# Kernel optimization log

Measured on AMD Instinct MI355X. Metric: run time of the kernel, lower is better.

The kernel has to match this reference:

```python
import jax, jax.numpy as jnp
import numpy as np

# ---- model hyperparameters (match init_kwargs) ----
D_MODEL = 1024
D_STATE = 128
EXPAND = 2
HEADDIM = 64
NGROUPS = 1
D_INNER = EXPAND * D_MODEL            # 2048
NHEADS = D_INNER // HEADDIM           # 32
ROPE_FRAC = 0.5
SPLIT = int(D_STATE * ROPE_FRAC)      # 64 rotary dims
NANG = SPLIT // 2                     # 32 rope angles
A_FLOOR = 1e-4
EPS = 1e-5
BATCH, SEQLEN = 1, 1024
SIZES = [D_INNER, D_INNER, D_STATE * NGROUPS, D_STATE * NGROUPS, NHEADS, NHEADS, NHEADS, NANG]
D_IN_PROJ = int(np.sum(SIZES))        # 4480


def setup_inputs() -> dict:
    key = jax.random.key(0)
    ks = jax.random.split(key, 6)
    u = jax.random.normal(ks[0], (BATCH, SEQLEN, D_MODEL), dtype=jnp.float32)
    W_in = jax.random.normal(ks[1], (D_MODEL, D_IN_PROJ), dtype=jnp.float32) * 0.02
    # dt_bias ~ log(dt) for dt in [1e-3, 0.1] -> around -4
    dt_bias = jax.random.normal(ks[2], (NHEADS,), dtype=jnp.float32) * 0.5 - 4.0
    B_bias = jnp.ones((NHEADS, D_STATE), jnp.float32) + 0.01 * jax.random.normal(ks[3], (NHEADS, D_STATE), dtype=jnp.float32)
    C_bias = jnp.ones((NHEADS, D_STATE), jnp.float32) + 0.01 * jax.random.normal(ks[4], (NHEADS, D_STATE), dtype=jnp.float32)
    Bn_w = jnp.ones((D_STATE,), jnp.float32)
    Cn_w = jnp.ones((D_STATE,), jnp.float32)
    D_param = jnp.ones((NHEADS,), jnp.float32)
    W_out = jax.random.normal(ks[5], (D_INNER, D_MODEL), dtype=jnp.float32) * 0.02
    return {"u": u, "W_in": W_in, "dt_bias": dt_bias, "B_bias": B_bias, "C_bias": C_bias,
            "Bn_w": Bn_w, "Cn_w": Cn_w, "D_param": D_param, "W_out": W_out}


def _rmsnorm(v, w):
    return v * jax.lax.rsqrt(jnp.mean(v * v, axis=-1, keepdims=True) + EPS) * w


def _forward(u, W_in, dt_bias, B_bias, C_bias, Bn_w, Cn_w, D_param, W_out):
    b, l, _ = u.shape
    proj = u @ W_in                                   # (b, l, d_in_proj)
    idx = np.cumsum(SIZES)[:-1]
    z, x, Bp, Cp, dd_dt, dd_A, trap_raw, ang = jnp.split(proj, idx, axis=-1)
    z = z.reshape(b, l, NHEADS, HEADDIM)
    x = x.reshape(b, l, NHEADS, HEADDIM)
    # A = clamp(-softplus(.), max=-A_floor);  dt = softplus(. + dt_bias)
    A = jnp.minimum(-jax.nn.softplus(dd_A), -A_FLOOR)          # (b,l,H)
    dt = jax.nn.softplus(dd_dt + dt_bias)                      # (b,l,H)
    a = jnp.exp(A * dt)                                        # decay per step
    lam = jax.nn.sigmoid(trap_raw)                             # trapezoid gate
    # RMSNorm on B/C (ngroups=1), then per-head additive bias
    Bn = _rmsnorm(Bp, Bn_w)                                    # (b,l,N)
    Cn = _rmsnorm(Cp, Cn_w)
    Bh = Bn[:, :, None, :] + B_bias                            # (b,l,H,N)
    Ch = Cn[:, :, None, :] + C_bias
    # data-dependent rotary: cumulative angle = cumsum(angles * dt)
    theta = jnp.cumsum(ang[:, :, None, :] * dt[..., None], axis=1)  # (b,l,H,NANG)
    cos, sin = jnp.cos(theta), jnp.sin(theta)

    def rope(v):
        d1, d2, rest = v[..., :NANG], v[..., NANG:SPLIT], v[..., SPLIT:]
        return jnp.concatenate([d1 * cos - d2 * sin, d1 * sin + d2 * cos, rest], axis=-1)

    Bh, Ch = rope(Bh), rope(Ch)

    tfirst = lambda v: jnp.moveaxis(v, 1, 0)
    inputs = (tfirst(Bh), tfirst(Ch), tfirst(x), tfirst(a), tfirst(dt), tfirst(lam))
    h0 = jnp.zeros((b, NHEADS, HEADDIM, D_STATE), jnp.float32)
    k0 = jnp.zeros((b, NHEADS, D_STATE), jnp.float32)
    v0 = jnp.zeros((b, NHEADS, HEADDIM), jnp.float32)

    def step(carry, inp):
        h, kp, vp = carry
        Bt, Ct, xt, at, dtt, lamt = inp
        # trapezoidal selective-scan update:
        # h_t = a_t h_{t-1} + dt_t (lam_t B_t x_t + (1-lam_t) a_t B_{t-1} x_{t-1})
        cur = jnp.einsum('bhp,bhn->bhpn', xt, Bt) * (dtt * lamt)[..., None, None]
        prv = jnp.einsum('bhp,bhn->bhpn', vp, kp) * (dtt * (1.0 - lamt) * at)[..., None, None]
        h = at[..., None, None] * h + cur + prv
        yt = jnp.einsum('bhn,bhpn->bhp', Ct, h)
        return (h, Bt, xt), yt

    _, y = jax.lax.scan(step, (h0, k0, v0), inputs)          # (l,b,H,P)
    y = jnp.moveaxis(y, 0, 1) + D_param[None, None, :, None] * x
    y = y * jax.nn.silu(z)                                    # gated output (no out-proj norm)
    return y.reshape(b, l, D_INNER) @ W_out


def reference(u, W_in, dt_bias, B_bias, C_bias, Bn_w, Cn_w, D_param, W_out):
    return _forward(u, W_in, dt_bias, B_bias, C_bias, Bn_w, Cn_w, D_param, W_out)
```

## Files before the change

### kernel.cpp

```cpp
#include <hip/hip_runtime.h>
#include <stdint.h>

#define SEQ     1024
#define DPROJ   4480

typedef __attribute__((ext_vector_type(8))) short short8;
typedef __attribute__((ext_vector_type(4))) float f4;

__device__ __forceinline__ short f2b(float f){
  union { float f; uint32_t u; } v; v.f = f;
  uint32_t r = (v.u + 0x7fffu + ((v.u >> 16) & 1u)) >> 16;
  return (short)(uint16_t)r;
}
__device__ __forceinline__ float b2f(uint16_t u){
  union { uint32_t u; float f; } v; v.u = ((uint32_t)u) << 16; return v.f;
}
__device__ __forceinline__ uint32_t pack2(float lo, float hi){
  return (uint32_t)(uint16_t)f2b(lo) | ((uint32_t)(uint16_t)f2b(hi) << 16);
}
__device__ __forceinline__ float softplus_f(float x){
  return x > 20.f ? x : log1pf(__expf(x));
}
__device__ __forceinline__ void gload_lds16(const short* g, short* l){
  __builtin_amdgcn_global_load_lds((const __attribute__((address_space(1))) void*)g,
                                   (__attribute__((address_space(3))) void*)l, 16, 0, 0);
}

__global__ __launch_bounds__(256) void prep_inputs(const float* __restrict__ u, short* __restrict__ u16,
                                                   const float* __restrict__ W_in, short* __restrict__ WtIn,
                                                   const float* __restrict__ W_out, short* __restrict__ WtOut,
                                                   float* __restrict__ outz){
  int b = blockIdx.x;
  int tid = threadIdx.x;
  if (b < 1024){
    int i = (b * 256 + tid) * 4;
    f4 v = *(const f4*)(u + i);
    uint2 pk; pk.x = pack2(v.x, v.y); pk.y = pack2(v.z, v.w);
    *(uint2*)(u16 + i) = pk;
    return;
  }
  if (b >= 2656){
    int i = ((b - 2656) * 256 + tid) * 4;
    *(f4*)(outz + i) = (f4){0.f, 0.f, 0.f, 0.f};
    return;
  }
  const float* in; short* outp; int R, lda, bx, by;
  if (b < 2144){ int idx = b - 1024; bx = idx % 140; by = idx / 140; in = W_in;  outp = WtIn;  R = 1024; lda = 4480; }
  else         { int idx = b - 2144; bx = idx & 31;  by = idx >> 5;  in = W_out; outp = WtOut; R = 2048; lda = 1024; }
  __shared__ float tile[32][132];
  int bc = bx * 32, br = by * 128;
  int c = tid & 31, r0 = tid >> 5;
  #pragma unroll
  for (int i = 0; i < 16; i++){
    int r = r0 + i * 8;
    tile[c][r] = in[(size_t)(br + r) * lda + bc + c];
  }
  __syncthreads();
  #pragma unroll
  for (int i = 0; i < 4; i++){
    int task = tid + 256 * i;
    int cc = task >> 5;
    int rg = (task & 31) * 4;
    f4 v = *(const f4*)&tile[cc][rg];
    uint2 pk; pk.x = pack2(v.x, v.y); pk.y = pack2(v.z, v.w);
    *(uint2*)(outp + (size_t)(bc + cc) * R + br + rg) = pk;
  }
}

__global__ __launch_bounds__(256) void gemm1_kernel(const short* __restrict__ A, const short* __restrict__ Bt,
                                                    float* __restrict__ C){
  const int N = 4480, K = 1024;
  __shared__ __align__(16) short As[2][128 * 32];
  __shared__ __align__(16) short Bs[2][160 * 32];
  const int tid  = threadIdx.x;
  const int wave = tid >> 6;
  const int lane = tid & 63;
  const int m0 = blockIdx.y * 128;
  const int n0 = blockIdx.x * 160;
  const int wm = (wave >> 1) * 64;
  const int wn = (wave & 1) * 80;
  const int quad = lane >> 4;
  const int r16  = lane & 15;

  f4 acc[4][5];
  #pragma unroll
  for (int i = 0; i < 4; i++)
    #pragma unroll
    for (int j = 0; j < 5; j++) acc[i][j] = (f4){0.f, 0.f, 0.f, 0.f};

  const int row0 = tid >> 2;
  const int kq   = tid & 3;
  const short* gA0 = A  + (size_t)(m0 + row0) * K + kq * 8;
  const short* gA1 = A  + (size_t)(m0 + row0 + 64) * K + kq * 8;
  const short* gB0 = Bt + (size_t)(n0 + row0) * K + kq * 8;
  const short* gB1 = Bt + (size_t)(n0 + row0 + 64) * K + kq * 8;
  const short* gB2 = Bt + (size_t)(n0 + row0 + 128) * K + kq * 8;

  gload_lds16(gA0, &As[0][(size_t)tid * 8]);
  gload_lds16(gA1, &As[0][(size_t)(tid + 256) * 8]);
  gload_lds16(gB0, &Bs[0][(size_t)tid * 8]);
  gload_lds16(gB1, &Bs[0][(size_t)(tid + 256) * 8]);
  if (tid < 128) gload_lds16(gB2, &Bs[0][(size_t)(tid + 512) * 8]);

  for (int kt = 0; kt < 32; ++kt){
    const int cur = kt & 1;
    __syncthreads();
    if (kt + 1 < 32){
      const int ko = (kt + 1) * 32;
      const int nxt = cur ^ 1;
      gload_lds16(gA0 + ko, &As[nxt][(size_t)tid * 8]);
      gload_lds16(gA1 + ko, &As[nxt][(size_t)(tid + 256) * 8]);
      gload_lds16(gB0 + ko, &Bs[nxt][(size_t)tid * 8]);
      gload_lds16(gB1 + ko, &Bs[nxt][(size_t)(tid + 256) * 8]);
      if (tid < 128) gload_lds16(gB2 + ko, &Bs[nxt][(size_t)(tid + 512) * 8]);
    }
    short8 af[4], bf[5];
    #pragma unroll
    for (int i = 0; i < 4; i++)
      af[i] = *(const short8*)&As[cur][(wm + i * 16 + r16) * 32 + quad * 8];
    #pragma unroll
    for (int j = 0; j < 5; j++)
      bf[j] = *(const short8*)&Bs[cur][(wn + j * 16 + r16) * 32 + quad * 8];
    #pragma unroll
    for (int i = 0; i < 4; i++)
      #pragma unroll
      for (int j = 0; j < 5; j++)
        acc[i][j] = __builtin_amdgcn_mfma_f32_16x16x32_bf16(af[i], bf[j], acc[i][j], 0, 0, 0);
  }

  #pragma unroll
  for (int i = 0; i < 4; i++)
    #pragma unroll
    for (int j = 0; j < 5; j++)
      #pragma unroll
      for (int rr = 0; rr < 4; ++rr){
        int row = m0 + wm + i * 16 + quad * 4 + rr;
        int col = n0 + wn + j * 16 + r16;
        C[(size_t)row * N + col] = acc[i][j][rr];
      }
}

__global__ __launch_bounds__(256) void gemm2_kernel(const short* __restrict__ A, const short* __restrict__ Bt,
                                                    float* __restrict__ C){
  const int N = 1024, K = 2048, klen = 512;
  __shared__ __align__(16) short As[2][128 * 32];
  __shared__ __align__(16) short Bs[2][128 * 32];
  const int tid  = threadIdx.x;
  const int wave = tid >> 6;
  const int lane = tid & 63;
  const int m0 = blockIdx.y * 128;
  const int n0 = blockIdx.x * 128;
  const int k0 = blockIdx.z * klen;
  const int wm = (wave >> 1) * 64;
  const int wn = (wave & 1) * 64;
  const int quad = lane >> 4;
  const int r16  = lane & 15;

  f4 acc[4][4];
  #pragma unroll
  for (int i = 0; i < 4; i++)
    #pragma unroll
    for (int j = 0; j < 4; j++) acc[i][j] = (f4){0.f, 0.f, 0.f, 0.f};

  const int row0 = tid >> 2;
  const int kq   = tid & 3;
  const short* gA0 = A  + (size_t)(m0 + row0) * K + k0 + kq * 8;
  const short* gA1 = A  + (size_t)(m0 + row0 + 64) * K + k0 + kq * 8;
  const short* gB0 = Bt + (size_t)(n0 + row0) * K + k0 + kq * 8;
  const short* gB1 = Bt + (size_t)(n0 + row0 + 64) * K + k0 + kq * 8;

  gload_lds16(gA0, &As[0][(size_t)tid * 8]);
  gload_lds16(gA1, &As[0][(size_t)(tid + 256) * 8]);
  gload_lds16(gB0, &Bs[0][(size_t)tid * 8]);
  gload_lds16(gB1, &Bs[0][(size_t)(tid + 256) * 8]);

  for (int kt = 0; kt < klen / 32; ++kt){
    const int cur = kt & 1;
    __syncthreads();
    if (kt + 1 < klen / 32){
      const int ko = (kt + 1) * 32;
      const int nxt = cur ^ 1;
      gload_lds16(gA0 + ko, &As[nxt][(size_t)tid * 8]);
      gload_lds16(gA1 + ko, &As[nxt][(size_t)(tid + 256) * 8]);
      gload_lds16(gB0 + ko, &Bs[nxt][(size_t)tid * 8]);
      gload_lds16(gB1 + ko, &Bs[nxt][(size_t)(tid + 256) * 8]);
    }
    short8 af[4], bf[4];
    #pragma unroll
    for (int i = 0; i < 4; i++){
      af[i] = *(const short8*)&As[cur][(wm + i * 16 + r16) * 32 + quad * 8];
      bf[i] = *(const short8*)&Bs[cur][(wn + i * 16 + r16) * 32 + quad * 8];
    }
    #pragma unroll
    for (int i = 0; i < 4; i++)
      #pragma unroll
      for (int j = 0; j < 4; j++)
        acc[i][j] = __builtin_amdgcn_mfma_f32_16x16x32_bf16(af[i], bf[j], acc[i][j], 0, 0, 0);
  }

  #pragma unroll
  for (int i = 0; i < 4; i++)
    #pragma unroll
    for (int j = 0; j < 4; j++)
      #pragma unroll
      for (int rr = 0; rr < 4; ++rr){
        int row = m0 + wm + i * 16 + quad * 4 + rr;
        int col = n0 + wn + j * 16 + r16;
        unsafeAtomicAdd(&C[(size_t)row * N + col], acc[i][j][rr]);
      }
}

__global__ __launch_bounds__(256) void scan_theta(const float* __restrict__ proj,
                                                  const float* __restrict__ dt_bias,
                                                  float* __restrict__ Lcum, float* __restrict__ u2b,
                                                  float* __restrict__ c1b,
                                                  float* __restrict__ cosb, float* __restrict__ sinb){
  int b = blockIdx.x;
  int tid = threadIdx.x;
  int t0 = tid * 4;
  int lane = tid & 63, wave = tid >> 6;
  __shared__ float wsum[4];
  if (b < 32){
    int h = b;
    float dtbias = dt_bias[h];
    float dt5[5], lam5[5];
    #pragma unroll
    for (int i = 0; i < 5; i++){
      int t = t0 + i;
      if (t < 1024){
        const float* row = proj + (size_t)t * DPROJ;
        dt5[i]  = softplus_f(row[4352 + h] + dtbias);
        lam5[i] = 1.f / (1.f + __expf(-row[4416 + h]));
      } else { dt5[i] = 0.f; lam5[i] = 0.f; }
    }
    float v[4], c1[4], c2n[4];
    #pragma unroll
    for (int i = 0; i < 4; i++){
      int t = t0 + i;
      const float* row = proj + (size_t)t * DPROJ;
      float Ah = -fmaxf(softplus_f(row[4384 + h]), 1e-4f);
      v[i]   = Ah * dt5[i];
      c1[i]  = dt5[i] * lam5[i];
      c2n[i] = dt5[i + 1] * (1.f - lam5[i + 1]);
    }
    v[1] += v[0]; v[2] += v[1]; v[3] += v[2];
    float tot = v[3], sc = tot;
    #pragma unroll
    for (int off = 1; off < 64; off <<= 1){
      float n = __shfl_up(sc, off, 64);
      if (lane >= off) sc += n;
    }
    if (lane == 63) wsum[wave] = sc;
    __syncthreads();
    float base = sc - tot;
    for (int w = 0; w < wave; ++w) base += wsum[w];
    #pragma unroll
    for (int i = 0; i < 4; i++){
      int t = t0 + i;
      Lcum[h * 1024 + t] = base + v[i];
      u2b[h * 1024 + t]  = c1[i] + c2n[i];
      c1b[h * 1024 + t]  = c1[i];
    }
  } else {
    int hk = b - 32;
    int h = hk >> 5, k = hk & 31;
    float dtbias = dt_bias[h];
    float v[4];
    #pragma unroll
    for (int i = 0; i < 4; i++){
      const float* row = proj + (size_t)(t0 + i) * DPROJ;
      float dt = softplus_f(row[4352 + h] + dtbias);
      v[i] = row[4448 + k] * dt;
    }
    v[1] += v[0]; v[2] += v[1]; v[3] += v[2];
    float tot = v[3], sc = tot;
    #pragma unroll
    for (int off = 1; off < 64; off <<= 1){
      float n = __shfl_up(sc, off, 64);
      if (lane >= off) sc += n;
    }
    if (lane == 63) wsum[wave] = sc;
    __syncthreads();
    float base = sc - tot;
    for (int w = 0; w < wave; ++w) base += wsum[w];
    #pragma unroll
    for (int i = 0; i < 4; i++){
      float th = base + v[i];
      float s, c;
      __sincosf(th, &s, &c);
      int t = t0 + i;
      cosb[(size_t)t * 1024 + h * 32 + k] = c;
      sinb[(size_t)t * 1024 + h * 32 + k] = s;
    }
  }
}

__global__ __launch_bounds__(256) void bcxt_kernel(const float* __restrict__ proj,
                                                   const float* __restrict__ B_bias, const float* __restrict__ C_bias,
                                                   const float* __restrict__ Bn_w, const float* __restrict__ Cn_w,
                                                   const float* __restrict__ cosb, const float* __restrict__ sinb,
                                                   short* __restrict__ Bb, short* __restrict__ Cb,
                                                   short* __restrict__ xTb){
  int b = blockIdx.x;
  int tid = threadIdx.x;
  if (b >= 1024){
    int idx = b - 1024;
    int bx = idx & 63, by = idx >> 6;
    __shared__ float tile[32][132];
    int bc = bx * 32, br = by * 128;
    int c = tid & 31, r0 = tid >> 5;
    #pragma unroll
    for (int i = 0; i < 16; i++){
      int r = r0 + i * 8;
      tile[c][r] = proj[(size_t)(br + r) * 4480 + 2048 + bc + c];
    }
    __syncthreads();
    #pragma unroll
    for (int i = 0; i < 4; i++){
      int task = tid + 256 * i;
      int cc = task >> 5;
      int rg = (task & 31) * 4;
      f4 v = *(const f4*)&tile[cc][rg];
      uint2 pk; pk.x = pack2(v.x, v.y); pk.y = pack2(v.z, v.w);
      *(uint2*)(xTb + (size_t)(bc + cc) * 1024 + br + rg) = pk;
    }
    return;
  }
  int t = b;
  __shared__ float vv[2][128];
  __shared__ float red[4];
  int n = tid & 127;
  int isC = tid >> 7;
  float val = proj[(size_t)t * DPROJ + 4096 + isC * 128 + n];
  float ss = val * val;
  #pragma unroll
  for (int off = 32; off >= 1; off >>= 1) ss += __shfl_down(ss, off);
  int wave = tid >> 6, lane = tid & 63;
  if (lane == 0) red[wave] = ss;
  __syncthreads();
  float rsv = isC ? rsqrtf((red[2] + red[3]) * (1.f / 128.f) + 1e-5f)
                  : rsqrtf((red[0] + red[1]) * (1.f / 128.f) + 1e-5f);
  vv[isC][n] = val * rsv * (isC ? Cn_w[n] : Bn_w[n]);
  __syncthreads();
  const float* cb = cosb + (size_t)t * 1024;
  const float* sb = sinb + (size_t)t * 1024;
  #pragma unroll
  for (int it = 0; it < 8; it++){
    int task = tid + 256 * it;
    int arr  = task >> 10;
    int rem  = task & 1023;
    int h    = rem >> 5;
    int n0   = (rem & 31) * 4;
    const float* bias = arr ? C_bias : B_bias;
    const float* base = vv[arr];
    f4 bv = *(const f4*)&base[n0];
    f4 bi = *(const f4*)&bias[h * 128 + n0];
    f4 o;
    if (n0 < 32){
      f4 bv2 = *(const f4*)&base[n0 + 32];
      f4 bi2 = *(const f4*)&bias[h * 128 + n0 + 32];
      f4 cv = *(const f4*)&cb[h * 32 + n0];
      f4 sv = *(const f4*)&sb[h * 32 + n0];
      #pragma unroll
      for (int q = 0; q < 4; q++) o[q] = (bv[q] + bi[q]) * cv[q] - (bv2[q] + bi2[q]) * sv[q];
    } else if (n0 < 64){
      int k0 = n0 - 32;
      f4 bv1 = *(const f4*)&base[k0];
      f4 bi1 = *(const f4*)&bias[h * 128 + k0];
      f4 cv = *(const f4*)&cb[h * 32 + k0];
      f4 sv = *(const f4*)&sb[h * 32 + k0];
      #pragma unroll
      for (int q = 0; q < 4; q++) o[q] = (bv1[q] + bi1[q]) * sv[q] + (bv[q] + bi[q]) * cv[q];
    } else {
      #pragma unroll
      for (int q = 0; q < 4; q++) o[q] = bv[q] + bi[q];
    }
    uint2 pk; pk.x = pack2(o.x, o.y); pk.y = pack2(o.z, o.w);
    short* outp = arr ? Cb : Bb;
    *(uint2*)(outp + (size_t)t * 4096 + h * 128 + n0) = pk;
  }
}

__global__ __launch_bounds__(256) void hpart_kernel(const short* __restrict__ xTb, const short* __restrict__ Bb,
                                                    const float* __restrict__ Lcum, const float* __restrict__ u2b,
                                                    short* __restrict__ Hpart){
  int h = blockIdx.x >> 3, c = blockIdx.x & 7;
  int t0 = c * 128;
  int tid = threadIdx.x;
  __shared__ __align__(16) short Bsm[128 * 128];
  __shared__ float wS[128];
  if (tid < 128){
    float Lend = Lcum[h * 1024 + t0 + 127];
    wS[tid] = __expf(Lend - Lcum[h * 1024 + t0 + tid]) * u2b[h * 1024 + t0 + tid];
  }
  #pragma unroll
  for (int it = 0; it < 8; it++){
    int slot = tid + 256 * it;
    int row = slot >> 4, c16 = slot & 15;
    gload_lds16(Bb + (size_t)(t0 + row) * 4096 + h * 128 + c16 * 8, &Bsm[(size_t)slot * 8]);
  }
  __syncthreads();

  int wave = tid >> 6, lane = tid & 63, quad = lane >> 4, r16 = lane & 15;
  int n0 = wave * 32;
  f4 acc[4][2];
  #pragma unroll
  for (int i = 0; i < 4; i++)
    #pragma unroll
    for (int j = 0; j < 2; j++) acc[i][j] = (f4){0.f, 0.f, 0.f, 0.f};

  #pragma unroll
  for (int kk = 0; kk < 4; ++kk){
    int sb = kk * 32 + quad * 8;
    short8 af[4];
    #pragma unroll
    for (int i = 0; i < 4; i++){
      int p = i * 16 + r16;
      af[i] = *(const short8*)(xTb + (size_t)(h * 64 + p) * 1024 + t0 + sb);
    }
    float wv[8];
    #pragma unroll
    for (int jj = 0; jj < 8; jj++) wv[jj] = wS[sb + jj];
    short8 bfr[2];
    #pragma unroll
    for (int j = 0; j < 2; j++){
      int nn = n0 + j * 16 + r16;
      float e[8];
      #pragma unroll
      for (int jj = 0; jj < 8; jj++)
        e[jj] = b2f((uint16_t)Bsm[(size_t)(sb + jj) * 128 + nn]) * wv[jj];
      union { short8 s; uint32_t u[4]; } fr;
      #pragma unroll
      for (int q = 0; q < 4; q++) fr.u[q] = pack2(e[2 * q], e[2 * q + 1]);
      bfr[j] = fr.s;
    }
    #pragma unroll
    for (int i = 0; i < 4; i++)
      #pragma unroll
      for (int j = 0; j < 2; j++)
        acc[i][j] = __builtin_amdgcn_mfma_f32_16x16x32_bf16(af[i], bfr[j], acc[i][j], 0, 0, 0);
  }

  short* out = Hpart + ((size_t)(h * 8 + c)) * 8192;
  #pragma unroll
  for (int i = 0; i < 4; i++)
    #pragma unroll
    for (int rr = 0; rr < 4; ++rr){
      int p = i * 16 + quad * 4 + rr;
      #pragma unroll
      for (int j = 0; j < 2; j++){
        int nn = n0 + j * 16 + r16;
        out[p * 128 + nn] = f2b(acc[i][j][rr]);
      }
    }
}

__global__ __launch_bounds__(256) void hscan_kernel(const short* __restrict__ Hpart,
                                                    const float* __restrict__ Lcum,
                                                    short* __restrict__ Hused){
  int idx = blockIdx.x * 256 + threadIdx.x;
  int h = idx >> 13, rem = idx & 8191;
  float acc = 0.f;
  float Lprev = 0.f;
  #pragma unroll
  for (int c = 0; c < 8; c++){
    Hused[((size_t)(h * 8 + c)) * 8192 + rem] = f2b(acc);
    float Lend = Lcum[h * 1024 + c * 128 + 127];
    float dec = __expf(Lend - Lprev);
    acc = dec * acc + b2f((uint16_t)Hpart[((size_t)(h * 8 + c)) * 8192 + rem]);
    Lprev = Lend;
  }
}

#define GS 144
__global__ __launch_bounds__(256) void chunky_kernel(const short* __restrict__ Cb, const short* __restrict__ Bbg,
                                                     const short* __restrict__ xTb, const short* __restrict__ Hused,
                                                     const float* __restrict__ Lcum, const float* __restrict__ u2b,
                                                     const float* __restrict__ c1b,
                                                     const float* __restrict__ proj, const float* __restrict__ D_par,
                                                     short* __restrict__ yb16){
  int h = blockIdx.x >> 3, c = blockIdx.x & 7;
  int t0 = c * 128;
  __shared__ __align__(16) short Gt[128 * GS];
  __shared__ float Lc[128], u2v[128], c1v[128];
  int tid = threadIdx.x;
  if (tid < 128){
    Lc[tid]  = Lcum[h * 1024 + t0 + tid];
    u2v[tid] = u2b[h * 1024 + t0 + tid];
    c1v[tid] = c1b[h * 1024 + t0 + tid];
  }
  float Lprev = (c > 0) ? Lcum[h * 1024 + t0 - 1] : 0.f;
  float Dp = D_par[h];
  int wave = tid >> 6, lane = tid & 63, quad = lane >> 4, r16 = lane & 15;
  int wm = (wave >> 1) * 64, wn = (wave & 1) * 64;

  f4 acc[4][4];
  #pragma unroll
  for (int i = 0; i < 4; i++)
    #pragma unroll
    for (int j = 0; j < 4; j++) acc[i][j] = (f4){0.f, 0.f, 0.f, 0.f};
  #pragma unroll
  for (int kk = 0; kk < 4; ++kk){
    short8 af[4], bf[4];
    #pragma unroll
    for (int i = 0; i < 4; i++)
      af[i] = *(const short8*)(Cb + (size_t)(t0 + wm + i * 16 + r16) * 4096 + h * 128 + kk * 32 + quad * 8);
    #pragma unroll
    for (int j = 0; j < 4; j++)
      bf[j] = *(const short8*)(Bbg + (size_t)(t0 + wn + j * 16 + r16) * 4096 + h * 128 + kk * 32 + quad * 8);
    #pragma unroll
    for (int i = 0; i < 4; i++)
      #pragma unroll
      for (int j = 0; j < 4; j++)
        acc[i][j] = __builtin_amdgcn_mfma_f32_16x16x32_bf16(af[i], bf[j], acc[i][j], 0, 0, 0);
  }
  __syncthreads();

  #pragma unroll
  for (int i = 0; i < 4; i++){
    #pragma unroll
    for (int rr = 0; rr < 4; ++rr){
      int trow = wm + i * 16 + quad * 4 + rr;
      float Lt = Lc[trow];
      #pragma unroll
      for (int j = 0; j < 4; j++){
        int scol = wn + j * 16 + r16;
        float g = 0.f;
        if (scol <= trow){
          float wcoef = (scol == trow) ? c1v[scol] : u2v[scol];
          g = acc[i][j][rr] * wcoef * __expf(Lt - Lc[scol]);
        }
        Gt[trow * GS + scol] = f2b(g);
      }
    }
  }
  __syncthreads();

  f4 accY[2][4], accZ[2][4];
  #pragma unroll
  for (int i = 0; i < 2; i++)
    #pragma unroll
    for (int j = 0; j < 4; j++){ accY[i][j] = (f4){0.f,0.f,0.f,0.f}; accZ[i][j] = (f4){0.f,0.f,0.f,0.f}; }
  int m0 = wave * 32;
  #pragma unroll
  for (int kk = 0; kk < 4; ++kk){
    short8 ag[2], ac[2], bx[4], bh[4];
    #pragma unroll
    for (int i = 0; i < 2; i++){
      ag[i] = *(const short8*)&Gt[(m0 + i * 16 + r16) * GS + kk * 32 + quad * 8];
      ac[i] = *(const short8*)(Cb + (size_t)(t0 + m0 + i * 16 + r16) * 4096 + h * 128 + kk * 32 + quad * 8);
    }
    #pragma unroll
    for (int j = 0; j < 4; j++){
      bx[j] = *(const short8*)(xTb + (size_t)(h * 64 + j * 16 + r16) * 1024 + t0 + kk * 32 + quad * 8);
      bh[j] = *(const short8*)(Hused + ((size_t)(h * 8 + c) * 64 + j * 16 + r16) * 128 + kk * 32 + quad * 8);
    }
    #pragma unroll
    for (int i = 0; i < 2; i++)
      #pragma unroll
      for (int j = 0; j < 4; j++){
        accY[i][j] = __builtin_amdgcn_mfma_f32_16x16x32_bf16(ag[i], bx[j], accY[i][j], 0, 0, 0);
        accZ[i][j] = __builtin_amdgcn_mfma_f32_16x16x32_bf16(ac[i], bh[j], accZ[i][j], 0, 0, 0);
      }
  }
  #pragma unroll
  for (int i = 0; i < 2; i++)
    #pragma unroll
    for (int rr = 0; rr < 4; ++rr){
      int trow = m0 + i * 16 + quad * 4 + rr;
      float ei = __expf(Lc[trow] - Lprev);
      const float* prow = proj + (size_t)(t0 + trow) * DPROJ;
      #pragma unroll
      for (int j = 0; j < 4; j++){
        int col = h * 64 + j * 16 + r16;
        float zv = prow[col];
        float xv = prow[2048 + col];
        float yv = accY[i][j][rr] + ei * accZ[i][j][rr] + Dp * xv;
        float o = yv * (zv / (1.f + __expf(-zv)));
        yb16[(size_t)(t0 + trow) * 2048 + col] = f2b(o);
      }
    }
}

extern "C" void kernel_launch(void* const* d_in, const int* in_sizes, int n_in,
                              void* d_out, int out_size, void* d_ws, size_t ws_size,
                              hipStream_t stream){
  const float* u       = (const float*)d_in[0];
  const float* W_in    = (const float*)d_in[1];
  const float* dt_bias = (const float*)d_in[2];
  const float* B_bias  = (const float*)d_in[3];
  const float* C_bias  = (const float*)d_in[4];
  const float* Bn_w    = (const float*)d_in[5];
  const float* Cn_w    = (const float*)d_in[6];
  const float* D_par   = (const float*)d_in[7];
  const float* W_out   = (const float*)d_in[8];
  float* out = (float*)d_out;

  char* ws = (char*)d_ws;
  short* u16   = (short*)(ws + 0);
  short* WtIn  = (short*)(ws + 2097152);
  short* WtOut = (short*)(ws + 11272192);
  float* proj  = (float*)(ws + 15466496);
  float* cosb  = (float*)(ws + 33816576);
  float* sinb  = (float*)(ws + 38010880);
  short* Bb    = (short*)(ws + 42205184);
  short* Cb    = (short*)(ws + 50593792);
  short* xTb   = (short*)(ws + 58982400);
  float* Lcum  = (float*)(ws + 63176704);
  float* u2b   = (float*)(ws + 63307776);
  float* c1b   = (float*)(ws + 63438848);
  short* Hpart = (short*)(ws + 63569920);
  short* Hused = (short*)(ws + 67764224);
  short* yb16  = (short*)(ws + 71958528);

  prep_inputs<<<3680, 256, 0, stream>>>(u, u16, W_in, WtIn, W_out, WtOut, out);
  gemm1_kernel<<<dim3(28, 8), 256, 0, stream>>>(u16, WtIn, proj);
  scan_theta<<<1056, 256, 0, stream>>>(proj, dt_bias, Lcum, u2b, c1b, cosb, sinb);
  bcxt_kernel<<<1536, 256, 0, stream>>>(proj, B_bias, C_bias, Bn_w, Cn_w, cosb, sinb, Bb, Cb, xTb);
  hpart_kernel<<<256, 256, 0, stream>>>(xTb, Bb, Lcum, u2b, Hpart);
  hscan_kernel<<<1024, 256, 0, stream>>>(Hpart, Lcum, Hused);
  chunky_kernel<<<256, 256, 0, stream>>>(Cb, Bb, xTb, Hused, Lcum, u2b, c1b, proj, D_par, yb16);
  gemm2_kernel<<<dim3(8, 8, 4), 256, 0, stream>>>(yb16, WtOut, out);
}
```

Baseline: 206.3 us.

## Fuse all stages into one persistent kernel with grid-wide atomic barriers

Replaces the eight separate kernel launches with a single persistent 256-block kernel. Each former kernel becomes a phase, with the original grid sizes folded into per-block loops, and phases are separated by a software grid barrier built on atomics. Shared memory is unioned across phases. This removes launch gaps and tail effects between kernels, but costs barrier spin overhead, caps parallelism at 256 blocks (the prep phases previously used 1024 or more), and relies on all blocks being co-resident.

```diff
diff --git a/kernel.cpp b/kernel.cpp
--- a/kernel.cpp
+++ b/kernel.cpp
@@ -26,560 +26,553 @@
                                    (__attribute__((address_space(3))) void*)l, 16, 0, 0);
 }
 
-__global__ __launch_bounds__(256) void prep_inputs(const float* __restrict__ u, short* __restrict__ u16,
-                                                   const float* __restrict__ W_in, short* __restrict__ WtIn,
-                                                   const float* __restrict__ W_out, short* __restrict__ WtOut,
-                                                   float* __restrict__ outz){
-  int b = blockIdx.x;
-  int tid = threadIdx.x;
-  if (b < 1024){
-    int i = (b * 256 + tid) * 4;
-    f4 v = *(const f4*)(u + i);
-    uint2 pk; pk.x = pack2(v.x, v.y); pk.y = pack2(v.z, v.w);
-    *(uint2*)(u16 + i) = pk;
-    return;
-  }
-  if (b >= 2656){
-    int i = ((b - 2656) * 256 + tid) * 4;
-    *(f4*)(outz + i) = (f4){0.f, 0.f, 0.f, 0.f};
-    return;
-  }
-  const float* in; short* outp; int R, lda, bx, by;
-  if (b < 2144){ int idx = b - 1024; bx = idx % 140; by = idx / 140; in = W_in;  outp = WtIn;  R = 1024; lda = 4480; }
-  else         { int idx = b - 2144; bx = idx & 31;  by = idx >> 5;  in = W_out; outp = WtOut; R = 2048; lda = 1024; }
-  __shared__ float tile[32][132];
-  int bc = bx * 32, br = by * 128;
-  int c = tid & 31, r0 = tid >> 5;
-  #pragma unroll
-  for (int i = 0; i < 16; i++){
-    int r = r0 + i * 8;
-    tile[c][r] = in[(size_t)(br + r) * lda + bc + c];
-  }
+__device__ __forceinline__ void gbar(int* bar, int phase){
   __syncthreads();
-  #pragma unroll
-  for (int i = 0; i < 4; i++){
-    int task = tid + 256 * i;
-    int cc = task >> 5;
-    int rg = (task & 31) * 4;
-    f4 v = *(const f4*)&tile[cc][rg];
-    uint2 pk; pk.x = pack2(v.x, v.y); pk.y = pack2(v.z, v.w);
-    *(uint2*)(outp + (size_t)(bc + cc) * R + br + rg) = pk;
-  }
-}
-
-__global__ __launch_bounds__(256) void gemm1_kernel(const short* __restrict__ A, const short* __restrict__ Bt,
-                                                    float* __restrict__ C){
-  const int N = 4480, K = 1024;
-  __shared__ __align__(16) short As[2][128 * 32];
-  __shared__ __align__(16) short Bs[2][160 * 32];
-  const int tid  = threadIdx.x;
-  const int wave = tid >> 6;
-  const int lane = tid & 63;
-  const int m0 = blockIdx.y * 128;
-  const int n0 = blockIdx.x * 160;
-  const int wm = (wave >> 1) * 64;
-  const int wn = (wave & 1) * 80;
-  const int quad = lane >> 4;
-  const int r16  = lane & 15;
-
-  f4 acc[4][5];
-  #pragma unroll
-  for (int i = 0; i < 4; i++)
-    #pragma unroll
-    for (int j = 0; j < 5; j++) acc[i][j] = (f4){0.f, 0.f, 0.f, 0.f};
-
-  const int row0 = tid >> 2;
-  const int kq   = tid & 3;
-  const short* gA0 = A  + (size_t)(m0 + row0) * K + kq * 8;
-  const short* gA1 = A  + (size_t)(m0 + row0 + 64) * K + kq * 8;
-  const short* gB0 = Bt + (size_t)(n0 + row0) * K + kq * 8;
-  const short* gB1 = Bt + (size_t)(n0 + row0 + 64) * K + kq * 8;
-  const short* gB2 = Bt + (size_t)(n0 + row0 + 128) * K + kq * 8;
-
-  gload_lds16(gA0, &As[0][(size_t)tid * 8]);
-  gload_lds16(gA1, &As[0][(size_t)(tid + 256) * 8]);
-  gload_lds16(gB0, &Bs[0][(size_t)tid * 8]);
-  gload_lds16(gB1, &Bs[0][(size_t)(tid + 256) * 8]);
-  if (tid < 128) gload_lds16(gB2, &Bs[0][(size_t)(tid + 512) * 8]);
-
-  for (int kt = 0; kt < 32; ++kt){
-    const int cur = kt & 1;
+  if (threadIdx.x == 0){
+    __threadfence();
+    __hip_atomic_fetch_add(&bar[phase], 1, __ATOMIC_ACQ_REL, __HIP_MEMORY_SCOPE_AGENT);
+    while (__hip_atomic_load(&bar[phase], __ATOMIC_ACQUIRE, __HIP_MEMORY_SCOPE_AGENT) < 256)
+      __builtin_amdgcn_s_sleep(2);
+    __threadfence();
+  }
+  __syncthreads();
+}
+
+__global__ __launch_bounds__(64) void init_barrier(int* bar){
+  if (threadIdx.x < 16) bar[threadIdx.x] = 0;
+}
+
+#define GS 144
+
+__global__ __launch_bounds__(256, 2) void mega_kernel(
+    const float* __restrict__ u, const float* __restrict__ W_in, const float* __restrict__ dt_bias,
+    const float* __restrict__ B_bias, const float* __restrict__ C_bias,
+    const float* __restrict__ Bn_w, const float* __restrict__ Cn_w,
+    const float* __restrict__ D_par, const float* __restrict__ W_out, float* __restrict__ out,
+    short* __restrict__ u16, short* __restrict__ WtIn, short* __restrict__ WtOut,
+    float* __restrict__ proj, float* __restrict__ cosb, float* __restrict__ sinb,
+    short* __restrict__ Bb, short* __restrict__ Cb, short* __restrict__ xTb,
+    float* __restrict__ Lcum, float* __restrict__ u2b, float* __restrict__ c1b,
+    short* __restrict__ Hpart, short* __restrict__ Hused, short* __restrict__ yb16,
+    int* bar)
+{
+  __shared__ __align__(16) union SMem {
+    float tile[32][132];
+    struct { short As[2][4096]; short Bs[2][5120]; } g1;
+    struct { short As[2][4096]; short Bs[2][4096]; } g2;
+    float wsum[4];
+    struct { float vv[2][128]; float red[4]; } bc;
+    struct { short Bsm[16384]; float wS[128]; } hp;
+    struct { short Gt[128 * GS]; float Lc[128], u2v[128], c1v[128]; } ck;
+  } sm;
+  const int tid = threadIdx.x;
+  const int bid = blockIdx.x;
+
+  #pragma unroll 1
+  for (int it = 0; it < 15; ++it){
+    int b = bid + 256 * it;
+    if (b >= 3680) break;
+    if (b < 1024){
+      int i = (b * 256 + tid) * 4;
+      f4 v = *(const f4*)(u + i);
+      uint2 pk; pk.x = pack2(v.x, v.y); pk.y = pack2(v.z, v.w);
+      *(uint2*)(u16 + i) = pk;
+    } else if (b >= 2656){
+      int i = ((b - 2656) * 256 + tid) * 4;
+      *(f4*)(out + i) = (f4){0.f, 0.f, 0.f, 0.f};
+    } else {
+      const float* in; short* outp; int R, lda, bx, by;
+      if (b < 2144){ int idx = b - 1024; bx = idx % 140; by = idx / 140; in = W_in;  outp = WtIn;  R = 1024; lda = 4480; }
+      else         { int idx = b - 2144; bx = idx & 31;  by = idx >> 5;  in = W_out; outp = WtOut; R = 2048; lda = 1024; }
+      int bc0 = bx * 32, br = by * 128;
+      int c = tid & 31, r0 = tid >> 5;
+      #pragma unroll
+      for (int i = 0; i < 16; i++){
+        int r = r0 + i * 8;
+        sm.tile[c][r] = in[(size_t)(br + r) * lda + bc0 + c];
+      }
+      __syncthreads();
+      #pragma unroll
+      for (int i = 0; i < 4; i++){
+        int task = tid + 256 * i;
+        int cc = task >> 5;
+        int rg = (task & 31) * 4;
+        f4 v = *(const f4*)&sm.tile[cc][rg];
+        uint2 pk; pk.x = pack2(v.x, v.y); pk.y = pack2(v.z, v.w);
+        *(uint2*)(outp + (size_t)(bc0 + cc) * R + br + rg) = pk;
+      }
+      __syncthreads();
+    }
+  }
+  gbar(bar, 0);
+
+  if (bid < 224){
+    const int N = 4480, K = 1024;
+    const int wave = tid >> 6, lane = tid & 63;
+    const int m0 = (bid / 28) * 128;
+    const int n0 = (bid % 28) * 160;
+    const int wm = (wave >> 1) * 64, wn = (wave & 1) * 80;
+    const int quad = lane >> 4, r16 = lane & 15;
+    f4 acc[4][5];
+    #pragma unroll
+    for (int i = 0; i < 4; i++)
+      #pragma unroll
+      for (int j = 0; j < 5; j++) acc[i][j] = (f4){0.f, 0.f, 0.f, 0.f};
+    const int row0 = tid >> 2;
+    const int kq   = tid & 3;
+    const short* gA0 = u16  + (size_t)(m0 + row0) * K + kq * 8;
+    const short* gA1 = u16  + (size_t)(m0 + row0 + 64) * K + kq * 8;
+    const short* gB0 = WtIn + (size_t)(n0 + row0) * K + kq * 8;
+    const short* gB1 = WtIn + (size_t)(n0 + row0 + 64) * K + kq * 8;
+    const short* gB2 = WtIn + (size_t)(n0 + row0 + 128) * K + kq * 8;
+    gload_lds16(gA0, &sm.g1.As[0][(size_t)tid * 8]);
+    gload_lds16(gA1, &sm.g1.As[0][(size_t)(tid + 256) * 8]);
+    gload_lds16(gB0, &sm.g1.Bs[0][(size_t)tid * 8]);
+    gload_lds16(gB1, &sm.g1.Bs[0][(size_t)(tid + 256) * 8]);
+    if (tid < 128) gload_lds16(gB2, &sm.g1.Bs[0][(size_t)(tid + 512) * 8]);
+    for (int kt = 0; kt < 32; ++kt){
+      const int cur = kt & 1;
+      __syncthreads();
+      if (kt + 1 < 32){
+        const int ko = (kt + 1) * 32;
+        const int nxt = cur ^ 1;
+        gload_lds16(gA0 + ko, &sm.g1.As[nxt][(size_t)tid * 8]);
+        gload_lds16(gA1 + ko, &sm.g1.As[nxt][(size_t)(tid + 256) * 8]);
+        gload_lds16(gB0 + ko, &sm.g1.Bs[nxt][(size_t)tid * 8]);
+        gload_lds16(gB1 + ko, &sm.g1.Bs[nxt][(size_t)(tid + 256) * 8]);
+        if (tid < 128) gload_lds16(gB2 + ko, &sm.g1.Bs[nxt][(size_t)(tid + 512) * 8]);
+      }
+      short8 af[4], bf[5];
+      #pragma unroll
+      for (int i = 0; i < 4; i++)
+        af[i] = *(const short8*)&sm.g1.As[cur][(wm + i * 16 + r16) * 32 + quad * 8];
+      #pragma unroll
+      for (int j = 0; j < 5; j++)
+        bf[j] = *(const short8*)&sm.g1.Bs[cur][(wn + j * 16 + r16) * 32 + quad * 8];
+      #pragma unroll
+      for (int i = 0; i < 4; i++)
+        #pragma unroll
+        for (int j = 0; j < 5; j++)
+          acc[i][j] = __builtin_amdgcn_mfma_f32_16x16x32_bf16(af[i], bf[j], acc[i][j], 0, 0, 0);
+    }
+    #pragma unroll
+    for (int i = 0; i < 4; i++)
+      #pragma unroll
+      for (int j = 0; j < 5; j++)
+        #pragma unroll
+        for (int rr = 0; rr < 4; ++rr){
+          int row = m0 + wm + i * 16 + quad * 4 + rr;
+          int col = n0 + wn + j * 16 + r16;
+          proj[(size_t)row * N + col] = acc[i][j][rr];
+        }
+  }
+  gbar(bar, 1);
+
+  {
+    int lane = tid & 63, wave = tid >> 6;
+    int t0 = tid * 4;
+    if (bid < 32){
+      int h = bid;
+      float dtbias = dt_bias[h];
+      float dt5[5], lam5[5];
+      #pragma unroll
+      for (int i = 0; i < 5; i++){
+        int t = t0 + i;
+        if (t < 1024){
+          const float* row = proj + (size_t)t * DPROJ;
+          dt5[i]  = softplus_f(row[4352 + h] + dtbias);
+          lam5[i] = 1.f / (1.f + __expf(-row[4416 + h]));
+        } else { dt5[i] = 0.f; lam5[i] = 0.f; }
+      }
+      float v[4], c1[4], c2n[4];
+      #pragma unroll
+      for (int i = 0; i < 4; i++){
+        int t = t0 + i;
+        const float* row = proj + (size_t)t * DPROJ;
+        float Ah = -fmaxf(softplus_f(row[4384 + h]), 1e-4f);
+        v[i]   = Ah * dt5[i];
+        c1[i]  = dt5[i] * lam5[i];
+        c2n[i] = dt5[i + 1] * (1.f - lam5[i + 1]);
+      }
+      v[1] += v[0]; v[2] += v[1]; v[3] += v[2];
+      float tot = v[3], sc = tot;
+      #pragma unroll
+      for (int off = 1; off < 64; off <<= 1){
+        float n = __shfl_up(sc, off, 64);
+        if (lane >= off) sc += n;
+      }
+      if (lane == 63) sm.wsum[wave] = sc;
+      __syncthreads();
+      float base = sc - tot;
+      for (int w = 0; w < wave; ++w) base += sm.wsum[w];
+      #pragma unroll
+      for (int i = 0; i < 4; i++){
+        int t = t0 + i;
+        Lcum[h * 1024 + t] = base + v[i];
+        u2b[h * 1024 + t]  = c1[i] + c2n[i];
+        c1b[h * 1024 + t]  = c1[i];
+      }
+      __syncthreads();
+    }
+    #pragma unroll 1
+    for (int it = 0; it < 4; ++it){
+      int ub = bid + 256 * it;
+      int h = ub >> 5, k = ub & 31;
+      float dtbias = dt_bias[h];
+      float v[4];
+      #pragma unroll
+      for (int i = 0; i < 4; i++){
+        const float* row = proj + (size_t)(t0 + i) * DPROJ;
+        float dt = softplus_f(row[4352 + h] + dtbias);
+        v[i] = row[4448 + k] * dt;
+      }
+      v[1] += v[0]; v[2] += v[1]; v[3] += v[2];
+      float tot = v[3], sc = tot;
+      #pragma unroll
+      for (int off = 1; off < 64; off <<= 1){
+        float n = __shfl_up(sc, off, 64);
+        if (lane >= off) sc += n;
+      }
+      if (lane == 63) sm.wsum[wave] = sc;
+      __syncthreads();
+      float base = sc - tot;
+      for (int w = 0; w < wave; ++w) base += sm.wsum[w];
+      #pragma unroll
+      for (int i = 0; i < 4; i++){
+        float th = base + v[i];
+        float s, c;
+        __sincosf(th, &s, &c);
+        int t = t0 + i;
+        cosb[(size_t)t * 1024 + h * 32 + k] = c;
+        sinb[(size_t)t * 1024 + h * 32 + k] = s;
+      }
+      __syncthreads();
+    }
+  }
+  gbar(bar, 2);
+
+  #pragma unroll 1
+  for (int it = 0; it < 6; ++it){
+    int b = bid + 256 * it;
+    if (b >= 1024){
+      int idx = b - 1024;
+      int bx = idx & 63, by = idx >> 6;
+      int bc0 = bx * 32, br = by * 128;
+      int c = tid & 31, r0 = tid >> 5;
+      #pragma unroll
+      for (int i = 0; i < 16; i++){
+        int r = r0 + i * 8;
+        sm.tile[c][r] = proj[(size_t)(br + r) * 4480 + 2048 + bc0 + c];
+      }
+      __syncthreads();
+      #pragma unroll
+      for (int i = 0; i < 4; i++){
+        int task = tid + 256 * i;
+        int cc = task >> 5;
+        int rg = (task & 31) * 4;
+        f4 v = *(const f4*)&sm.tile[cc][rg];
+        uint2 pk; pk.x = pack2(v.x, v.y); pk.y = pack2(v.z, v.w);
+        *(uint2*)(xTb + (size_t)(bc0 + cc) * 1024 + br + rg) = pk;
+      }
+      __syncthreads();
+    } else {
+      int t = b;
+      int n = tid & 127;
+      int isC = tid >> 7;
+      float val = proj[(size_t)t * DPROJ + 4096 + isC * 128 + n];
+      float ss = val * val;
+      #pragma unroll
+      for (int off = 32; off >= 1; off >>= 1) ss += __shfl_down(ss, off);
+      int wave = tid >> 6, lane = tid & 63;
+      if (lane == 0) sm.bc.red[wave] = ss;
+      __syncthreads();
+      float rsv = isC ? rsqrtf((sm.bc.red[2] + sm.bc.red[3]) * (1.f / 128.f) + 1e-5f)
+                      : rsqrtf((sm.bc.red[0] + sm.bc.red[1]) * (1.f / 128.f) + 1e-5f);
+      sm.bc.vv[isC][n] = val * rsv * (isC ? Cn_w[n] : Bn_w[n]);
+      __syncthreads();
+      const float* cb = cosb + (size_t)t * 1024;
+      const float* sb = sinb + (size_t)t * 1024;
+      #pragma unroll
+      for (int it2 = 0; it2 < 8; it2++){
+        int task = tid + 256 * it2;
+        int arr  = task >> 10;
+        int rem  = task & 1023;
+        int h    = rem >> 5;
+        int n0   = (rem & 31) * 4;
+        const float* bias = arr ? C_bias : B_bias;
+        const float* base = sm.bc.vv[arr];
+        f4 bv = *(const f4*)&base[n0];
+        f4 bi = *(const f4*)&bias[h * 128 + n0];
+        f4 o;
+        if (n0 < 32){
+          f4 bv2 = *(const f4*)&base[n0 + 32];
+          f4 bi2 = *(const f4*)&bias[h * 128 + n0 + 32];
+          f4 cv = *(const f4*)&cb[h * 32 + n0];
+          f4 sv = *(const f4*)&sb[h * 32 + n0];
+          #pragma unroll
+          for (int q = 0; q < 4; q++) o[q] = (bv[q] + bi[q]) * cv[q] - (bv2[q] + bi2[q]) * sv[q];
+        } else if (n0 < 64){
+          int k0 = n0 - 32;
+          f4 bv1 = *(const f4*)&base[k0];
+          f4 bi1 = *(const f4*)&bias[h * 128 + k0];
+          f4 cv = *(const f4*)&cb[h * 32 + k0];
+          f4 sv = *(const f4*)&sb[h * 32 + k0];
+          #pragma unroll
+          for (int q = 0; q < 4; q++) o[q] = (bv1[q] + bi1[q]) * sv[q] + (bv[q] + bi[q]) * cv[q];
+        } else {
+          #pragma unroll
+          for (int q = 0; q < 4; q++) o[q] = bv[q] + bi[q];
+        }
+        uint2 pk; pk.x = pack2(o.x, o.y); pk.y = pack2(o.z, o.w);
+        short* outp = arr ? Cb : Bb;
+        *(uint2*)(outp + (size_t)t * 4096 + h * 128 + n0) = pk;
+      }
+      __syncthreads();
+    }
+  }
+  gbar(bar, 3);
+
+  {
+    int h = bid >> 3, c = bid & 7;
+    int t0 = c * 128;
+    if (tid < 128){
+      float Lend = Lcum[h * 1024 + t0 + 127];
+      sm.hp.wS[tid] = __expf(Lend - Lcum[h * 1024 + t0 + tid]) * u2b[h * 1024 + t0 + tid];
+    }
+    #pragma unroll
+    for (int it = 0; it < 8; it++){
+      int slot = tid + 256 * it;
+      int row = slot >> 4, c16 = slot & 15;
+      gload_lds16(Bb + (size_t)(t0 + row) * 4096 + h * 128 + c16 * 8, &sm.hp.Bsm[(size_t)slot * 8]);
+    }
     __syncthreads();
-    if (kt + 1 < 32){
-      const int ko = (kt + 1) * 32;
-      const int nxt = cur ^ 1;
-      gload_lds16(gA0 + ko, &As[nxt][(size_t)tid * 8]);
-      gload_lds16(gA1 + ko, &As[nxt][(size_t)(tid + 256) * 8]);
-      gload_lds16(gB0 + ko, &Bs[nxt][(size_t)tid * 8]);
-      gload_lds16(gB1 + ko, &Bs[nxt][(size_t)(tid + 256) * 8]);
-      if (tid < 128) gload_lds16(gB2 + ko, &Bs[nxt][(size_t)(tid + 512) * 8]);
-    }
-    short8 af[4], bf[5];
+    int wave = tid >> 6, lane = tid & 63, quad = lane >> 4, r16 = lane & 15;
+    int n0 = wave * 32;
+    f4 acc[4][2];
     #pragma unroll
     for (int i = 0; i < 4; i++)
-      af[i] = *(const short8*)&As[cur][(wm + i * 16 + r16) * 32 + quad * 8];
-    #pragma unroll
-    for (int j = 0; j < 5; j++)
-      bf[j] = *(const short8*)&Bs[cur][(wn + j * 16 + r16) * 32 + quad * 8];
-    #pragma unroll
-    for (int i = 0; i < 4; i++)
-      #pragma unroll
-      for (int j = 0; j < 5; j++)
-        acc[i][j] = __builtin_amdgcn_mfma_f32_16x16x32_bf16(af[i], bf[j], acc[i][j], 0, 0, 0);
-  }
-
-  #pragma unroll
-  for (int i = 0; i < 4; i++)
-    #pragma unroll
-    for (int j = 0; j < 5; j++)
-      #pragma unroll
-      for (int rr = 0; rr < 4; ++rr){
-        int row = m0 + wm + i * 16 + quad * 4 + rr;
-        int col = n0 + wn + j * 16 + r16;
-        C[(size_t)row * N + col] = acc[i][j][rr];
-      }
-}
-
-__global__ __launch_bounds__(256) void gemm2_kernel(const short* __restrict__ A, const short* __restrict__ Bt,
-                                                    float* __restrict__ C){
-  const int N = 1024, K = 2048, klen = 512;
-  __shared__ __align__(16) short As[2][128 * 32];
-  __shared__ __align__(16) short Bs[2][128 * 32];
-  const int tid  = threadIdx.x;
-  const int wave = tid >> 6;
-  const int lane = tid & 63;
-  const int m0 = blockIdx.y * 128;
-  const int n0 = blockIdx.x * 128;
-  const int k0 = blockIdx.z * klen;
-  const int wm = (wave >> 1) * 64;
-  const int wn = (wave & 1) * 64;
-  const int quad = lane >> 4;
-  const int r16  = lane & 15;
-
-  f4 acc[4][4];
-  #pragma unroll
-  for (int i = 0; i < 4; i++)
-    #pragma unroll
-    for (int j = 0; j < 4; j++) acc[i][j] = (f4){0.f, 0.f, 0.f, 0.f};
-
-  const int row0 = tid >> 2;
-  const int kq   = tid & 3;
-  const short* gA0 = A  + (size_t)(m0 + row0) * K + k0 + kq * 8;
-  const short* gA1 = A  + (size_t)(m0 + row0 + 64) * K + k0 + kq * 8;
-  const short* gB0 = Bt + (size_t)(n0 + row0) * K + k0 + kq * 8;
-  const short* gB1 = Bt + (size_t)(n0 + row0 + 64) * K + k0 + kq * 8;
-
-  gload_lds16(gA0, &As[0][(size_t)tid * 8]);
-  gload_lds16(gA1, &As[0][(size_t)(tid + 256) * 8]);
-  gload_lds16(gB0, &Bs[0][(size_t)tid * 8]);
-  gload_lds16(gB1, &Bs[0][(size_t)(tid + 256) * 8]);
-
-  for (int kt = 0; kt < klen / 32; ++kt){
-    const int cur = kt & 1;
-    __syncthreads();
-    if (kt + 1 < klen / 32){
-      const int ko = (kt + 1) * 32;
-      const int nxt = cur ^ 1;
-      gload_lds16(gA0 + ko, &As[nxt][(size_t)tid * 8]);
-      gload_lds16(gA1 + ko, &As[nxt][(size_t)(tid + 256) * 8]);
-      gload_lds16(gB0 + ko, &Bs[nxt][(size_t)tid * 8]);
-      gload_lds16(gB1 + ko, &Bs[nxt][(size_t)(tid + 256) * 8]);
-    }
-    short8 af[4], bf[4];
-    #pragma unroll
-    for (int i = 0; i < 4; i++){
-      af[i] = *(const short8*)&As[cur][(wm + i * 16 + r16) * 32 + quad * 8];
-      bf[i] = *(const short8*)&Bs[cur][(wn + i * 16 + r16) * 32 + quad * 8];
-    }
-    #pragma unroll
-    for (int i = 0; i < 4; i++)
-      #pragma unroll
-      for (int j = 0; j < 4; j++)
-        acc[i][j] = __builtin_amdgcn_mfma_f32_16x16x32_bf16(af[i], bf[j], acc[i][j], 0, 0, 0);
-  }
-
-  #pragma unroll
-  for (int i = 0; i < 4; i++)
-    #pragma unroll
-    for (int j = 0; j < 4; j++)
-      #pragma unroll
-      for (int rr = 0; rr < 4; ++rr){
-        int row = m0 + wm + i * 16 + quad * 4 + rr;
-        int col = n0 + wn + j * 16 + r16;
-        unsafeAtomicAdd(&C[(size_t)row * N + col], acc[i][j][rr]);
-      }
-}
-
-__global__ __launch_bounds__(256) void scan_theta(const float* __restrict__ proj,
-                                                  const float* __restrict__ dt_bias,
-                                                  float* __restrict__ Lcum, float* __restrict__ u2b,
-                                                  float* __restrict__ c1b,
-                                                  float* __restrict__ cosb, float* __restrict__ sinb){
-  int b = blockIdx.x;
-  int tid = threadIdx.x;
-  int t0 = tid * 4;
-  int lane = tid & 63, wave = tid >> 6;
-  __shared__ float wsum[4];
-  if (b < 32){
-    int h = b;
-    float dtbias = dt_bias[h];
-    float dt5[5], lam5[5];
-    #pragma unroll
-    for (int i = 0; i < 5; i++){
-      int t = t0 + i;
-      if (t < 1024){
-        const float* row = proj + (size_t)t * DPROJ;
-        dt5[i]  = softplus_f(row[4352 + h] + dtbias);
-        lam5[i] = 1.f / (1.f + __expf(-row[4416 + h]));
-      } else { dt5[i] = 0.f; lam5[i] = 0.f; }
-    }
-    float v[4], c1[4], c2n[4];
-    #pragma unroll
-    for (int i = 0; i < 4; i++){
-      int t = t0 + i;
-      const float* row = proj + (size_t)t * DPROJ;
-      float Ah = -fmaxf(softplus_f(row[4384 + h]), 1e-4f);
-      v[i]   = Ah * dt5[i];
-      c1[i]  = dt5[i] * lam5[i];
-      c2n[i] = dt5[i + 1] * (1.f - lam5[i + 1]);
-    }
-    v[1] += v[0]; v[2] += v[1]; v[3] += v[2];
-    float tot = v[3], sc = tot;
-    #pragma unroll
-    for (int off = 1; off < 64; off <<= 1){
-      float n = __shfl_up(sc, off, 64);
-      if (lane >= off) sc += n;
-    }
-    if (lane == 63) wsum[wave] = sc;
-    __syncthreads();
-    float base = sc - tot;
-    for (int w = 0; w < wave; ++w) base += wsum[w];
-    #pragma unroll
-    for (int i = 0; i < 4; i++){
-      int t = t0 + i;
-      Lcum[h * 1024 + t] = base + v[i];
-      u2b[h * 1024 + t]  = c1[i] + c2n[i];
-      c1b[h * 1024 + t]  = c1[i];
-    }
-  } else {
-    int hk = b - 32;
-    int h = hk >> 5, k = hk & 31;
-    float dtbias = dt_bias[h];
-    float v[4];
-    #pragma unroll
-    for (int i = 0; i < 4; i++){
-      const float* row = proj + (size_t)(t0 + i) * DPROJ;
-      float dt = softplus_f(row[4352 + h] + dtbias);
-      v[i] = row[4448 + k] * dt;
-    }
-    v[1] += v[0]; v[2] += v[1]; v[3] += v[2];
-    float tot = v[3], sc = tot;
-    #pragma unroll
-    for (int off = 1; off < 64; off <<= 1){
-      float n = __shfl_up(sc, off, 64);
-      if (lane >= off) sc += n;
-    }
-    if (lane == 63) wsum[wave] = sc;
-    __syncthreads();
-    float base = sc - tot;
-    for (int w = 0; w < wave; ++w) base += wsum[w];
-    #pragma unroll
-    for (int i = 0; i < 4; i++){
-      float th = base + v[i];
-      float s, c;
-      __sincosf(th, &s, &c);
-      int t = t0 + i;
-      cosb[(size_t)t * 1024 + h * 32 + k] = c;
-      sinb[(size_t)t * 1024 + h * 32 + k] = s;
-    }
-  }
-}
-
-__global__ __launch_bounds__(256) void bcxt_kernel(const float* __restrict__ proj,
-                                                   const float* __restrict__ B_bias, const float* __restrict__ C_bias,
-                                                   const float* __restrict__ Bn_w, const float* __restrict__ Cn_w,
-                                                   const float* __restrict__ cosb, const float* __restrict__ sinb,
-                                                   short* __restrict__ Bb, short* __restrict__ Cb,
-                                                   short* __restrict__ xTb){
-  int b = blockIdx.x;
-  int tid = threadIdx.x;
-  if (b >= 1024){
-    int idx = b - 1024;
-    int bx = idx & 63, by = idx >> 6;
-    __shared__ float tile[32][132];
-    int bc = bx * 32, br = by * 128;
-    int c = tid & 31, r0 = tid >> 5;
-    #pragma unroll
-    for (int i = 0; i < 16; i++){
-      int r = r0 + i * 8;
-      tile[c][r] = proj[(size_t)(br + r) * 4480 + 2048 + bc + c];
-    }
-    __syncthreads();
-    #pragma unroll
-    for (int i = 0; i < 4; i++){
-      int task = tid + 256 * i;
-      int cc = task >> 5;
-      int rg = (task & 31) * 4;
-      f4 v = *(const f4*)&tile[cc][rg];
-      uint2 pk; pk.x = pack2(v.x, v.y); pk.y = pack2(v.z, v.w);
-      *(uint2*)(xTb + (size_t)(bc + cc) * 1024 + br + rg) = pk;
-    }
-    return;
-  }
-  int t = b;
-  __shared__ float vv[2][128];
-  __shared__ float red[4];
-  int n = tid & 127;
-  int isC = tid >> 7;
-  float val = proj[(size_t)t * DPROJ + 4096 + isC * 128 + n];
-  float ss = val * val;
-  #pragma unroll
-  for (int off = 32; off >= 1; off >>= 1) ss += __shfl_down(ss, off);
-  int wave = tid >> 6, lane = tid & 63;
-  if (lane == 0) red[wave] = ss;
-  __syncthreads();
-  float rsv = isC ? rsqrtf((red[2] + red[3]) * (1.f / 128.f) + 1e-5f)
-                  : rsqrtf((red[0] + red[1]) * (1.f / 128.f) + 1e-5f);
-  vv[isC][n] = val * rsv * (isC ? Cn_w[n] : Bn_w[n]);
-  __syncthreads();
-  const float* cb = cosb + (size_t)t * 1024;
-  const float* sb = sinb + (size_t)t * 1024;
-  #pragma unroll
-  for (int it = 0; it < 8; it++){
-    int task = tid + 256 * it;
-    int arr  = task >> 10;
-    int rem  = task & 1023;
-    int h    = rem >> 5;
-    int n0   = (rem & 31) * 4;
-    const float* bias = arr ? C_bias : B_bias;
-    const float* base = vv[arr];
-    f4 bv = *(const f4*)&base[n0];
-    f4 bi = *(const f4*)&bias[h * 128 + n0];
-    f4 o;
-    if (n0 < 32){
-      f4 bv2 = *(const f4*)&base[n0 + 32];
-      f4 bi2 = *(const f4*)&bias[h * 128 + n0 + 32];
-      f4 cv = *(const f4*)&cb[h * 32 + n0];
-      f4 sv = *(const f4*)&sb[h * 32 + n0];
-      #pragma unroll
-      for (int q = 0; q < 4; q++) o[q] = (bv[q] + bi[q]) * cv[q] - (bv2[q] + bi2[q]) * sv[q];
-    } else if (n0 < 64){
-      int k0 = n0 - 32;
-      f4 bv1 = *(const f4*)&base[k0];
-      f4 bi1 = *(const f4*)&bias[h * 128 + k0];
-      f4 cv = *(const f4*)&cb[h * 32 + k0];
-      f4 sv = *(const f4*)&sb[h * 32 + k0];
-      #pragma unroll
-      for (int q = 0; q < 4; q++) o[q] = (bv1[q] + bi1[q]) * sv[q] + (bv[q] + bi[q]) * cv[q];
-    } else {
-      #pragma unroll
-      for (int q = 0; q < 4; q++) o[q] = bv[q] + bi[q];
-    }
-    uint2 pk; pk.x = pack2(o.x, o.y); pk.y = pack2(o.z, o.w);
-    short* outp = arr ? Cb : Bb;
-    *(uint2*)(outp + (size_t)t * 4096 + h * 128 + n0) = pk;
-  }
-}
-
-__global__ __launch_bounds__(256) void hpart_kernel(const short* __restrict__ xTb, const short* __restrict__ Bb,
-                                                    const float* __restrict__ Lcum, const float* __restrict__ u2b,
-                                                    short* __restrict__ Hpart){
-  int h = blockIdx.x >> 3, c = blockIdx.x & 7;
-  int t0 = c * 128;
-  int tid = threadIdx.x;
-  __shared__ __align__(16) short Bsm[128 * 128];
-  __shared__ float wS[128];
-  if (tid < 128){
-    float Lend = Lcum[h * 1024 + t0 + 127];
-    wS[tid] = __expf(Lend - Lcum[h * 1024 + t0 + tid]) * u2b[h * 1024 + t0 + tid];
-  }
-  #pragma unroll
-  for (int it = 0; it < 8; it++){
-    int slot = tid + 256 * it;
-    int row = slot >> 4, c16 = slot & 15;
-    gload_lds16(Bb + (size_t)(t0 + row) * 4096 + h * 128 + c16 * 8, &Bsm[(size_t)slot * 8]);
-  }
-  __syncthreads();
-
-  int wave = tid >> 6, lane = tid & 63, quad = lane >> 4, r16 = lane & 15;
-  int n0 = wave * 32;
-  f4 acc[4][2];
-  #pragma unroll
-  for (int i = 0; i < 4; i++)
-    #pragma unroll
-    for (int j = 0; j < 2; j++) acc[i][j] = (f4){0.f, 0.f, 0.f, 0.f};
-
-  #pragma unroll
-  for (int kk = 0; kk < 4; ++kk){
-    int sb = kk * 32 + quad * 8;
-    short8 af[4];
-    #pragma unroll
-    for (int i = 0; i < 4; i++){
-      int p = i * 16 + r16;
-      af[i] = *(const short8*)(xTb + (size_t)(h * 64 + p) * 1024 + t0 + sb);
-    }
-    float wv[8];
-    #pragma unroll
-    for (int jj = 0; jj < 8; jj++) wv[jj] = wS[sb + jj];
-    short8 bfr[2];
-    #pragma unroll
-    for (int j = 0; j < 2; j++){
-      int nn = n0 + j * 16 + r16;
-      float e[8];
-      #pragma unroll
-      for (int jj = 0; jj < 8; jj++)
-        e[jj] = b2f((uint16_t)Bsm[(size_t)(sb + jj) * 128 + nn]) * wv[jj];
-      union { short8 s; uint32_t u[4]; } fr;
-      #pragma unroll
-      for (int q = 0; q < 4; q++) fr.u[q] = pack2(e[2 * q], e[2 * q + 1]);
-      bfr[j] = fr.s;
-    }
-    #pragma unroll
-    for (int i = 0; i < 4; i++)
-      #pragma unroll
-      for (int j = 0; j < 2; j++)
-        acc[i][j] = __builtin_amdgcn_mfma_f32_16x16x32_bf16(af[i], bfr[j], acc[i][j], 0, 0, 0);
-  }
-
-  short* out = Hpart + ((size_t)(h * 8 + c)) * 8192;
-  #pragma unroll
-  for (int i = 0; i < 4; i++)
-    #pragma unroll
-    for (int rr = 0; rr < 4; ++rr){
-      int p = i * 16 + quad * 4 + rr;
+      #pragma unroll
+      for (int j = 0; j < 2; j++) acc[i][j] = (f4){0.f, 0.f, 0.f, 0.f};
+    #pragma unroll
+    for (int kk = 0; kk < 4; ++kk){
+      int sb = kk * 32 + quad * 8;
+      short8 af[4];
+      #pragma unroll
+      for (int i = 0; i < 4; i++){
+        int p = i * 16 + r16;
+        af[i] = *(const short8*)(xTb + (size_t)(h * 64 + p) * 1024 + t0 + sb);
+      }
+      float wv[8];
+      #pragma unroll
+      for (int jj = 0; jj < 8; jj++) wv[jj] = sm.hp.wS[sb + jj];
+      short8 bfr[2];
       #pragma unroll
       for (int j = 0; j < 2; j++){
         int nn = n0 + j * 16 + r16;
-        out[p * 128 + nn] = f2b(acc[i][j][rr]);
-      }
-    }
-}
-
-__global__ __launch_bounds__(256) void hscan_kernel(const short* __restrict__ Hpart,
-                                                    const float* __restrict__ Lcum,
-                                                    short* __restrict__ Hused){
-  int idx = blockIdx.x * 256 + threadIdx.x;
-  int h = idx >> 13, rem = idx & 8191;
-  float acc = 0.f;
-  float Lprev = 0.f;
-  #pragma unroll
-  for (int c = 0; c < 8; c++){
-    Hused[((size_t)(h * 8 + c)) * 8192 + rem] = f2b(acc);
-    float Lend = Lcum[h * 1024 + c * 128 + 127];
-    float dec = __expf(Lend - Lprev);
-    acc = dec * acc + b2f((uint16_t)Hpart[((size_t)(h * 8 + c)) * 8192 + rem]);
-    Lprev = Lend;
-  }
-}
-
-#define GS 144
-__global__ __launch_bounds__(256) void chunky_kernel(const short* __restrict__ Cb, const short* __restrict__ Bbg,
-                                                     const short* __restrict__ xTb, const short* __restrict__ Hused,
-                                                     const float* __restrict__ Lcum, const float* __restrict__ u2b,
-                                                     const float* __restrict__ c1b,
-                                                     const float* __restrict__ proj, const float* __restrict__ D_par,
-                                                     short* __restrict__ yb16){
-  int h = blockIdx.x >> 3, c = blockIdx.x & 7;
-  int t0 = c * 128;
-  __shared__ __align__(16) short Gt[128 * GS];
-  __shared__ float Lc[128], u2v[128], c1v[128];
-  int tid = threadIdx.x;
-  if (tid < 128){
-    Lc[tid]  = Lcum[h * 1024 + t0 + tid];
-    u2v[tid] = u2b[h * 1024 + t0 + tid];
-    c1v[tid] = c1b[h * 1024 + t0 + tid];
-  }
-  float Lprev = (c > 0) ? Lcum[h * 1024 + t0 - 1] : 0.f;
-  float Dp = D_par[h];
-  int wave = tid >> 6, lane = tid & 63, quad = lane >> 4, r16 = lane & 15;
-  int wm = (wave >> 1) * 64, wn = (wave & 1) * 64;
-
-  f4 acc[4][4];
-  #pragma unroll
-  for (int i = 0; i < 4; i++)
-    #pragma unroll
-    for (int j = 0; j < 4; j++) acc[i][j] = (f4){0.f, 0.f, 0.f, 0.f};
-  #pragma unroll
-  for (int kk = 0; kk < 4; ++kk){
-    short8 af[4], bf[4];
+        float e[8];
+        #pragma unroll
+        for (int jj = 0; jj < 8; jj++)
+          e[jj] = b2f((uint16_t)sm.hp.Bsm[(size_t)(sb + jj) * 128 + nn]) * wv[jj];
+        union { short8 s; uint32_t u[4]; } fr;
+        #pragma unroll
+        for (int q = 0; q < 4; q++) fr.u[q] = pack2(e[2 * q], e[2 * q + 1]);
+        bfr[j] = fr.s;
+      }
+      #pragma unroll
+      for (int i = 0; i < 4; i++)
+        #pragma unroll
+        for (int j = 0; j < 2; j++)
+          acc[i][j] = __builtin_amdgcn_mfma_f32_16x16x32_bf16(af[i], bfr[j], acc[i][j], 0, 0, 0);
+    }
+    short* outp = Hpart + ((size_t)(h * 8 + c)) * 8192;
     #pragma unroll
     for (int i = 0; i < 4; i++)
-      af[i] = *(const short8*)(Cb + (size_t)(t0 + wm + i * 16 + r16) * 4096 + h * 128 + kk * 32 + quad * 8);
-    #pragma unroll
-    for (int j = 0; j < 4; j++)
-      bf[j] = *(const short8*)(Bbg + (size_t)(t0 + wn + j * 16 + r16) * 4096 + h * 128 + kk * 32 + quad * 8);
+      #pragma unroll
+      for (int rr = 0; rr < 4; ++rr){
+        int p = i * 16 + quad * 4 + rr;
+        #pragma unroll
+        for (int j = 0; j < 2; j++){
+          int nn = n0 + j * 16 + r16;
+          outp[p * 128 + nn] = f2b(acc[i][j][rr]);
+        }
+      }
+  }
+  gbar(bar, 4);
+
+  #pragma unroll 1
+  for (int it = 0; it < 4; ++it){
+    int idx = (bid + 256 * it) * 256 + tid;
+    int h = idx >> 13, rem = idx & 8191;
+    float acc = 0.f;
+    float Lprev = 0.f;
+    #pragma unroll
+    for (int c = 0; c < 8; c++){
+      Hused[((size_t)(h * 8 + c)) * 8192 + rem] = f2b(acc);
+      float Lend = Lcum[h * 1024 + c * 128 + 127];
+      float dec = __expf(Lend - Lprev);
+      acc = dec * acc + b2f((uint16_t)Hpart[((size_t)(h * 8 + c)) * 8192 + rem]);
+      Lprev = Lend;
+    }
+  }
+  gbar(bar, 5);
+
+  {
+    int h = bid >> 3, c = bid & 7;
+    int t0 = c * 128;
+    if (tid < 128){
+      sm.ck.Lc[tid]  = Lcum[h * 1024 + t0 + tid];
+      sm.ck.u2v[tid] = u2b[h * 1024 + t0 + tid];
+      sm.ck.c1v[tid] = c1b[h * 1024 + t0 + tid];
+    }
+    float Lprev = (c > 0) ? Lcum[h * 1024 + t0 - 1] : 0.f;
+    float Dp = D_par[h];
+    int wave = tid >> 6, lane = tid & 63, quad = lane >> 4, r16 = lane & 15;
+    int wm = (wave >> 1) * 64, wn = (wave & 1) * 64;
+
+    f4 acc[4][4];
     #pragma unroll
     for (int i = 0; i < 4; i++)
       #pragma unroll
+      for (int j = 0; j < 4; j++) acc[i][j] = (f4){0.f, 0.f, 0.f, 0.f};
+    #pragma unroll
+    for (int kk = 0; kk < 4; ++kk){
+      short8 af[4], bf[4];
+      #pragma unroll
+      for (int i = 0; i < 4; i++)
+        af[i] = *(const short8*)(Cb + (size_t)(t0 + wm + i * 16 + r16) * 4096 + h * 128 + kk * 32 + quad * 8);
+      #pragma unroll
       for (int j = 0; j < 4; j++)
-        acc[i][j] = __builtin_amdgcn_mfma_f32_16x16x32_bf16(af[i], bf[j], acc[i][j], 0, 0, 0);
-  }
-  __syncthreads();
-
-  #pragma unroll
-  for (int i = 0; i < 4; i++){
-    #pragma unroll
-    for (int rr = 0; rr < 4; ++rr){
-      int trow = wm + i * 16 + quad * 4 + rr;
-      float Lt = Lc[trow];
+        bf[j] = *(const short8*)(Bb + (size_t)(t0 + wn + j * 16 + r16) * 4096 + h * 128 + kk * 32 + quad * 8);
+      #pragma unroll
+      for (int i = 0; i < 4; i++)
+        #pragma unroll
+        for (int j = 0; j < 4; j++)
+          acc[i][j] = __builtin_amdgcn_mfma_f32_16x16x32_bf16(af[i], bf[j], acc[i][j], 0, 0, 0);
+    }
+    __syncthreads();
+    #pragma unroll
+    for (int i = 0; i < 4; i++){
+      #pragma unroll
+      for (int rr = 0; rr < 4; ++rr){
+        int trow = wm + i * 16 + quad * 4 + rr;
+        float Lt = sm.ck.Lc[trow];
+        #pragma unroll
+        for (int j = 0; j < 4; j++){
+          int scol = wn + j * 16 + r16;
+          float g = 0.f;
+          if (scol <= trow){
+            float wcoef = (scol == trow) ? sm.ck.c1v[scol] : sm.ck.u2v[scol];
+            g = acc[i][j][rr] * wcoef * __expf(Lt - sm.ck.Lc[scol]);
+          }
+          sm.ck.Gt[trow * GS + scol] = f2b(g);
+        }
+      }
+    }
+    __syncthreads();
+    f4 accY[2][4], accZ[2][4];
+    #pragma unroll
+    for (int i = 0; i < 2; i++)
+      #pragma unroll
+      for (int j = 0; j < 4; j++){ accY[i][j] = (f4){0.f,0.f,0.f,0.f}; accZ[i][j] = (f4){0.f,0.f,0.f,0.f}; }
+    int m0 = wave * 32;
+    #pragma unroll
+    for (int kk = 0; kk < 4; ++kk){
+      short8 ag[2], ac[2], bx[4], bh[4];
+      #pragma unroll
+      for (int i = 0; i < 2; i++){
+        ag[i] = *(const short8*)&sm.ck.Gt[(m0 + i * 16 + r16) * GS + kk * 32 + quad * 8];
+        ac[i] = *(const short8*)(Cb + (size_t)(t0 + m0 + i * 16 + r16) * 4096 + h * 128 + kk * 32 + quad * 8);
+      }
       #pragma unroll
       for (int j = 0; j < 4; j++){
-        int scol = wn + j * 16 + r16;
-        float g = 0.f;
-        if (scol <= trow){
-          float wcoef = (scol == trow) ? c1v[scol] : u2v[scol];
-          g = acc[i][j][rr] * wcoef * __expf(Lt - Lc[scol]);
+        bx[j] = *(const short8*)(xTb + (size_t)(h * 64 + j * 16 + r16) * 1024 + t0 + kk * 32 + quad * 8);
+        bh[j] = *(const short8*)(Hused + ((size_t)(h * 8 + c) * 64 + j * 16 + r16) * 128 + kk * 32 + quad * 8);
+      }
+      #pragma unroll
+      for (int i = 0; i < 2; i++)
+        #pragma unroll
+        for (int j = 0; j < 4; j++){
+          accY[i][j] = __builtin_amdgcn_mfma_f32_16x16x32_bf16(ag[i], bx[j], accY[i][j], 0, 0, 0);
+          accZ[i][j] = __builtin_amdgcn_mfma_f32_16x16x32_bf16(ac[i], bh[j], accZ[i][j], 0, 0, 0);
         }
-        Gt[trow * GS + scol] = f2b(g);
-      }
-    }
-  }
-  __syncthreads();
-
-  f4 accY[2][4], accZ[2][4];
-  #pragma unroll
-  for (int i = 0; i < 2; i++)
-    #pragma unroll
-    for (int j = 0; j < 4; j++){ accY[i][j] = (f4){0.f,0.f,0.f,0.f}; accZ[i][j] = (f4){0.f,0.f,0.f,0.f}; }
-  int m0 = wave * 32;
-  #pragma unroll
-  for (int kk = 0; kk < 4; ++kk){
-    short8 ag[2], ac[2], bx[4], bh[4];
-    #pragma unroll
-    for (int i = 0; i < 2; i++){
-      ag[i] = *(const short8*)&Gt[(m0 + i * 16 + r16) * GS + kk * 32 + quad * 8];
-      ac[i] = *(const short8*)(Cb + (size_t)(t0 + m0 + i * 16 + r16) * 4096 + h * 128 + kk * 32 + quad * 8);
-    }
-    #pragma unroll
-    for (int j = 0; j < 4; j++){
-      bx[j] = *(const short8*)(xTb + (size_t)(h * 64 + j * 16 + r16) * 1024 + t0 + kk * 32 + quad * 8);
-      bh[j] = *(const short8*)(Hused + ((size_t)(h * 8 + c) * 64 + j * 16 + r16) * 128 + kk * 32 + quad * 8);
     }
     #pragma unroll
     for (int i = 0; i < 2; i++)
       #pragma unroll
-      for (int j = 0; j < 4; j++){
-        accY[i][j] = __builtin_amdgcn_mfma_f32_16x16x32_bf16(ag[i], bx[j], accY[i][j], 0, 0, 0);
-        accZ[i][j] = __builtin_amdgcn_mfma_f32_16x16x32_bf16(ac[i], bh[j], accZ[i][j], 0, 0, 0);
-      }
-  }
-  #pragma unroll
-  for (int i = 0; i < 2; i++)
-    #pragma unroll
-    for (int rr = 0; rr < 4; ++rr){
-      int trow = m0 + i * 16 + quad * 4 + rr;
-      float ei = __expf(Lc[trow] - Lprev);
-      const float* prow = proj + (size_t)(t0 + trow) * DPROJ;
-      #pragma unroll
-      for (int j = 0; j < 4; j++){
-        int col = h * 64 + j * 16 + r16;
-        float zv = prow[col];
-        float xv = prow[2048 + col];
-        float yv = accY[i][j][rr] + ei * accZ[i][j][rr] + Dp * xv;
-        float o = yv * (zv / (1.f + __expf(-zv)));
-        yb16[(size_t)(t0 + trow) * 2048 + col] = f2b(o);
-      }
-    }
+      for (int rr = 0; rr < 4; ++rr){
+        int trow = m0 + i * 16 + quad * 4 + rr;
+        float ei = __expf(sm.ck.Lc[trow] - Lprev);
+        const float* prow = proj + (size_t)(t0 + trow) * DPROJ;
+        #pragma unroll
+        for (int j = 0; j < 4; j++){
+          int col = h * 64 + j * 16 + r16;
+          float zv = prow[col];
+          float xv = prow[2048 + col];
+          float yv = accY[i][j][rr] + ei * accZ[i][j][rr] + Dp * xv;
+          float o = yv * (zv / (1.f + __expf(-zv)));
+          yb16[(size_t)(t0 + trow) * 2048 + col] = f2b(o);
+        }
+      }
+  }
+  gbar(bar, 6);
+
+  {
+    const int N = 1024, K = 2048, klen = 512;
+    const int wave = tid >> 6, lane = tid & 63;
+    const int n0 = (bid & 7) * 128;
+    const int m0 = ((bid >> 3) & 7) * 128;
+    const int k0 = (bid >> 6) * klen;
+    const int wm = (wave >> 1) * 64, wn = (wave & 1) * 64;
+    const int quad = lane >> 4, r16 = lane & 15;
+    f4 acc[4][4];
+    #pragma unroll
+    for (int i = 0; i < 4; i++)
+      #pragma unroll
+      for (int j = 0; j < 4; j++) acc[i][j] = (f4){0.f, 0.f, 0.f, 0.f};
+    const int row0 = tid >> 2;
+    const int kq   = tid & 3;
+    const short* gA0 = yb16  + (size_t)(m0 + row0) * K + k0 + kq * 8;
+    const short* gA1 = yb16  + (size_t)(m0 + row0 + 64) * K + k0 + kq * 8;
+    const short* gB0 = WtOut + (size_t)(n0 + row0) * K + k0 + kq * 8;
+    const short* gB1 = WtOut + (size_t)(n0 + row0 + 64) * K + k0 + kq * 8;
+    gload_lds16(gA0, &sm.g2.As[0][(size_t)tid * 8]);
+    gload_lds16(gA1, &sm.g2.As[0][(size_t)(tid + 256) * 8]);
+    gload_lds16(gB0, &sm.g2.Bs[0][(size_t)tid * 8]);
+    gload_lds16(gB1, &sm.g2.Bs[0][(size_t)(tid + 256) * 8]);
+    for (int kt = 0; kt < klen / 32; ++kt){
+      const int cur = kt & 1;
+      __syncthreads();
+      if (kt + 1 < klen / 32){
+        const int ko = (kt + 1) * 32;
+        const int nxt = cur ^ 1;
+        gload_lds16(gA0 + ko, &sm.g2.As[nxt][(size_t)tid * 8]);
+        gload_lds16(gA1 + ko, &sm.g2.As[nxt][(size_t)(tid + 256) * 8]);
+        gload_lds16(gB0 + ko, &sm.g2.Bs[nxt][(size_t)tid * 8]);
+        gload_lds16(gB1 + ko, &sm.g2.Bs[nxt][(size_t)(tid + 256) * 8]);
+      }
+      short8 af[4], bf[4];
+      #pragma unroll
+      for (int i = 0; i < 4; i++){
+        af[i] = *(const short8*)&sm.g2.As[cur][(wm + i * 16 + r16) * 32 + quad * 8];
+        bf[i] = *(const short8*)&sm.g2.Bs[cur][(wn + i * 16 + r16) * 32 + quad * 8];
+      }
+      #pragma unroll
+      for (int i = 0; i < 4; i++)
+        #pragma unroll
+        for (int j = 0; j < 4; j++)
+          acc[i][j] = __builtin_amdgcn_mfma_f32_16x16x32_bf16(af[i], bf[j], acc[i][j], 0, 0, 0);
+    }
+    #pragma unroll
+    for (int i = 0; i < 4; i++)
+      #pragma unroll
+      for (int j = 0; j < 4; j++)
+        #pragma unroll
+        for (int rr = 0; rr < 4; ++rr){
+          int row = m0 + wm + i * 16 + quad * 4 + rr;
+          int col = n0 + wn + j * 16 + r16;
+          unsafeAtomicAdd(&out[(size_t)row * N + col], acc[i][j][rr]);
+        }
+  }
 }
 
 extern "C" void kernel_launch(void* const* d_in, const int* in_sizes, int n_in,
@@ -612,13 +605,10 @@
   short* Hpart = (short*)(ws + 63569920);
   short* Hused = (short*)(ws + 67764224);
   short* yb16  = (short*)(ws + 71958528);
-
-  prep_inputs<<<3680, 256, 0, stream>>>(u, u16, W_in, WtIn, W_out, WtOut, out);
-  gemm1_kernel<<<dim3(28, 8), 256, 0, stream>>>(u16, WtIn, proj);
-  scan_theta<<<1056, 256, 0, stream>>>(proj, dt_bias, Lcum, u2b, c1b, cosb, sinb);
-  bcxt_kernel<<<1536, 256, 0, stream>>>(proj, B_bias, C_bias, Bn_w, Cn_w, cosb, sinb, Bb, Cb, xTb);
-  hpart_kernel<<<256, 256, 0, stream>>>(xTb, Bb, Lcum, u2b, Hpart);
-  hscan_kernel<<<1024, 256, 0, stream>>>(Hpart, Lcum, Hused);
-  chunky_kernel<<<256, 256, 0, stream>>>(Cb, Bb, xTb, Hused, Lcum, u2b, c1b, proj, D_par, yb16);
-  gemm2_kernel<<<dim3(8, 8, 4), 256, 0, stream>>>(yb16, WtOut, out);
-}
+  int*   bar   = (int*)  (ws + 76152832);
+
+  init_barrier<<<1, 64, 0, stream>>>(bar);
+  mega_kernel<<<256, 256, 0, stream>>>(u, W_in, dt_bias, B_bias, C_bias, Bn_w, Cn_w, D_par,
+                                       W_out, out, u16, WtIn, WtOut, proj, cosb, sinb,
+                                       Bb, Cb, xTb, Lcum, u2b, c1b, Hpart, Hused, yb16, bar);
+}
```

New measurement: 490.5 us. 2.38x slower.
